# Performance work log

Measured on AMD Instinct MI355X. Metric: run time of the kernel, lower is better.

The kernel has to match this reference:

```python
import jax, jax.numpy as jnp
import numpy as np

EPS = 1e-3  # Keras BatchNormalization default epsilon


def _bn(x, gamma, beta, mean, var):
    # inference-mode batchnorm over channel axis 1 of [N,C,T,V]
    s = (gamma * jax.lax.rsqrt(var + EPS)).reshape(1, -1, 1, 1)
    b = (beta - gamma * mean * jax.lax.rsqrt(var + EPS)).reshape(1, -1, 1, 1)
    return x * s + b


def setup_inputs() -> dict:
    key = jax.random.key(0)
    ks = jax.random.split(key, 10)
    N, C, T, V, K, F, KT = 64, 64, 300, 25, 3, 64, 9
    x = jax.random.normal(ks[0], (N, C, T, V), jnp.float32)
    W1 = jax.random.normal(ks[1], (C, F * K), jnp.float32) * 0.05
    b1 = jnp.zeros((F * K,), jnp.float32)
    A = jax.random.normal(ks[2], (K, T, V, V), jnp.float32) * 0.2
    gamma1 = jnp.ones((F,), jnp.float32)
    beta1 = jnp.zeros((F,), jnp.float32)
    mean1 = jax.random.normal(ks[3], (F,), jnp.float32) * 0.1
    var1 = jax.random.uniform(ks[4], (F,), jnp.float32) + 0.5
    Wt = jax.random.normal(ks[5], (KT, 1, F, F), jnp.float32) * 0.05  # HWIO
    bt = jnp.zeros((F,), jnp.float32)
    gamma2 = jnp.ones((F,), jnp.float32)
    beta2 = jnp.zeros((F,), jnp.float32)
    mean2 = jax.random.normal(ks[6], (F,), jnp.float32) * 0.1
    var2 = jax.random.uniform(ks[7], (F,), jnp.float32) + 0.5
    return dict(x=x, W1=W1, b1=b1, A=A, gamma1=gamma1, beta1=beta1,
                mean1=mean1, var1=var1, Wt=Wt, bt=bt, gamma2=gamma2,
                beta2=beta2, mean2=mean2, var2=var2)


def reference(x, W1, b1, A, gamma1, beta1, mean1, var1, Wt, bt,
              gamma2, beta2, mean2, var2):
    N, C, T, V = x.shape
    K = A.shape[0]
    F = W1.shape[1] // K
    # SGTACN: 1x1 conv (channels_first) == channel matmul
    y = jnp.einsum('nctv,cf->nftv', x, W1) + b1.reshape(1, -1, 1, 1)
    y = y.reshape(N, K, F, T, V)
    # spatial graph contraction with learned per-timestep adjacency
    y = jnp.einsum('nkftv,ktvw->nftw', y, A)
    # tgcn: BN -> relu -> temporal conv [9,1] SAME -> BN
    y = jax.nn.relu(_bn(y, gamma1, beta1, mean1, var1))
    y = jax.lax.conv_general_dilated(
        y, Wt, window_strides=(1, 1), padding='SAME',
        dimension_numbers=('NCHW', 'HWIO', 'NCHW')) + bt.reshape(1, -1, 1, 1)
    y = _bn(y, gamma2, beta2, mean2, var2)
    # identity residual (stride=1, no downsample, C_in == filters) + relu
    return jax.nn.relu(y + x)
```

## Files before the change

### kernel.cpp

```cpp
#include <hip/hip_runtime.h>
#include <hip/hip_bf16.h>
#include <stdint.h>

#define EPS 1e-3f

typedef __attribute__((ext_vector_type(8))) short bf16x8;
typedef __attribute__((ext_vector_type(4))) float f32x4;

__device__ inline uint32_t pk2(float a, float b) {
    __hip_bfloat162 p;
    p.x = __float2bfloat16(a);
    p.y = __float2bfloat16(b);
    return *(uint32_t*)&p;
}

__global__ __launch_bounds__(256) void k0_prep_small(
    const float* __restrict__ W1, const float* __restrict__ Wt,
    const float* __restrict__ A,
    uint16_t* __restrict__ W1t, uint16_t* __restrict__ Abf,
    float* __restrict__ csA_g)
{
    int i = blockIdx.x * 256 + threadIdx.x;
    if (i < 12288) {
        int f = i / 192, Kp = i % 192, k = Kp >> 6, c = Kp & 63;
        __hip_bfloat16 b = __float2bfloat16(W1[c * 192 + k * 64 + f]);
        W1t[i] = *(uint16_t*)&b;
    } else if (i < 49152) {
        int j = i - 12288;
        int jj = j & 7, fo = (j >> 3) & 63, kb = j >> 9;
        int kk = kb * 8 + jj, dt = kk >> 6, fi = kk & 63;
        __hip_bfloat16 b = __float2bfloat16(Wt[(dt * 64 + fi) * 64 + fo]);
        Abf[j] = *(uint16_t*)&b;
    } else if (i < 71652) {
        int j = i - 49152;
        int k = j / 7500, r = j % 7500;
        int t = r / 25, w = r % 25;
        float s = 0.f;
        for (int v = 0; v < 25; ++v)
            s += A[((k * 300 + t) * 25 + v) * 25 + w];
        csA_g[j] = s;
    }
}

__global__ __launch_bounds__(256) void k0_prep_At(
    const float* __restrict__ A, uint16_t* __restrict__ At_g)
{
    int i = blockIdx.x * 256 + threadIdx.x;
    if (i < 921600) {
        int v = i & 31, w = (i >> 5) & 31, rest = i >> 10;
        int t = rest % 300, k = rest / 300;
        float val = 0.f;
        if (v < 25 && w < 25)
            val = A[((k * 300 + t) * 25 + v) * 25 + w];
        __hip_bfloat16 b = __float2bfloat16(val);
        At_g[i] = *(uint16_t*)&b;
    }
}

#define K1_SMEM 39680
__global__ __launch_bounds__(256, 4) void k1_wave(
    const float* __restrict__ x, const uint16_t* __restrict__ At_g,
    const uint16_t* __restrict__ W1t, const float* __restrict__ csA_g,
    const float* __restrict__ b1,
    const float* __restrict__ gamma1, const float* __restrict__ beta1,
    const float* __restrict__ mean1, const float* __restrict__ var1,
    uint32_t* __restrict__ h2u)
{
    extern __shared__ __align__(16) char smem[];
    float* s1s   = (float*)(smem + 38400);
    float* b1ns  = (float*)(smem + 38656);
    float* b1s   = (float*)(smem + 38912);

    const int t0   = blockIdx.x * 4;
    const int n    = blockIdx.y;
    const int tid  = threadIdx.x;
    const int lane = tid & 63, wv = tid >> 6;
    const int l15  = lane & 15, g = lane >> 4;
    const int t    = t0 + wv;
    char* slab = smem + wv * 9600;

    bf16x8 bfr[6];
    #pragma unroll
    for (int nf = 0; nf < 6; ++nf) {
        const int col = nf * 16 + l15;
        const int k = col >> 5, w = col & 31;
        bfr[nf] = *(const bf16x8*)(At_g + (((k * 300 + t) * 32 + w) * 32 + g * 8));
    }

    const float* xb = x + (size_t)n * 480000 + t * 25;
    bf16x8 a[4];
    #pragma unroll
    for (int mf = 0; mf < 4; ++mf) {
        const int c = l15 + 16 * mf;
        const float* xr = xb + (size_t)c * 7500;
        union { bf16x8 v; uint32_t u[4]; } ua;
        if (g < 3) {
            const float* p = xr + g * 8;
            ua.u[0] = pk2(p[0], p[1]);
            ua.u[1] = pk2(p[2], p[3]);
            ua.u[2] = pk2(p[4], p[5]);
            ua.u[3] = pk2(p[6], p[7]);
        } else {
            ua.u[0] = pk2(xr[24], 0.f);
            ua.u[1] = 0; ua.u[2] = 0; ua.u[3] = 0;
        }
        a[mf] = ua.v;
    }

    if (tid < 64) {
        float rs = rsqrtf(var1[tid] + EPS);
        s1s[tid]  = gamma1[tid] * rs;
        b1ns[tid] = beta1[tid] - gamma1[tid] * mean1[tid] * rs;
    }
    if (tid >= 64 && tid < 256) b1s[tid - 64] = b1[tid - 64];
    __syncthreads();

    #pragma unroll
    for (int hh = 0; hh < 2; ++hh) {
        f32x4 acc[4][3];
        #pragma unroll
        for (int mf = 0; mf < 4; ++mf)
            #pragma unroll
            for (int nf3 = 0; nf3 < 3; ++nf3)
                acc[mf][nf3] = (f32x4){0.f, 0.f, 0.f, 0.f};

        #pragma unroll
        for (int nf3 = 0; nf3 < 3; ++nf3) {
            const int nf = hh * 3 + nf3;
            acc[0][nf3] = __builtin_amdgcn_mfma_f32_16x16x32_bf16(a[0], bfr[nf], acc[0][nf3], 0, 0, 0);
            acc[1][nf3] = __builtin_amdgcn_mfma_f32_16x16x32_bf16(a[1], bfr[nf], acc[1][nf3], 0, 0, 0);
            acc[2][nf3] = __builtin_amdgcn_mfma_f32_16x16x32_bf16(a[2], bfr[nf], acc[2][nf3], 0, 0, 0);
            acc[3][nf3] = __builtin_amdgcn_mfma_f32_16x16x32_bf16(a[3], bfr[nf], acc[3][nf3], 0, 0, 0);
        }

        #pragma unroll
        for (int nf3 = 0; nf3 < 3; ++nf3) {
            const int col = (hh * 3 + nf3) * 16 + l15;
            const int k = col >> 5, w = col & 31;
            if (w < 25) {
                const int sw = (w & 7) << 4;
                #pragma unroll
                for (int mf = 0; mf < 4; ++mf) {
                    const int c0 = mf * 16 + g * 4;
                    const int off = w * 384 + (((k * 64 + c0) * 2) ^ sw);
                    uint2 val;
                    val.x = pk2(acc[mf][nf3][0], acc[mf][nf3][1]);
                    val.y = pk2(acc[mf][nf3][2], acc[mf][nf3][3]);
                    *(uint2*)(slab + off) = val;
                }
            }
        }
    }

    asm volatile("s_waitcnt lgkmcnt(0)" ::: "memory");
    __builtin_amdgcn_sched_barrier(0);

    int wq[2], qaddr[2], qswz[2];
    #pragma unroll
    for (int q = 0; q < 2; ++q) {
        int w = q * 16 + l15;
        wq[q] = w;
        int wc = (w < 25) ? w : 24;
        qaddr[q] = wc * 384;
        qswz[q]  = (wc & 7) << 4;
    }

    f32x4 accz[4][2];
    #pragma unroll
    for (int mf = 0; mf < 4; ++mf)
        #pragma unroll
        for (int q = 0; q < 2; ++q)
            accz[mf][q] = (f32x4){0.f, 0.f, 0.f, 0.f};

    #pragma unroll
    for (int kb = 0; kb < 6; ++kb) {
        bf16x8 az[4];
        #pragma unroll
        for (int mf = 0; mf < 4; ++mf)
            az[mf] = *(const bf16x8*)(W1t + (l15 + 16 * mf) * 192 + kb * 32 + g * 8);
        #pragma unroll
        for (int q = 0; q < 2; ++q) {
            bf16x8 b = *(const bf16x8*)(slab + qaddr[q] + ((kb * 64 + g * 16) ^ qswz[q]));
            accz[0][q] = __builtin_amdgcn_mfma_f32_16x16x32_bf16(az[0], b, accz[0][q], 0, 0, 0);
            accz[1][q] = __builtin_amdgcn_mfma_f32_16x16x32_bf16(az[1], b, accz[1][q], 0, 0, 0);
            accz[2][q] = __builtin_amdgcn_mfma_f32_16x16x32_bf16(az[2], b, accz[2][q], 0, 0, 0);
            accz[3][q] = __builtin_amdgcn_mfma_f32_16x16x32_bf16(az[3], b, accz[3][q], 0, 0, 0);
        }
    }

    const uint32_t tb = (uint32_t)(n * 300 + t);
    #pragma unroll
    for (int q = 0; q < 2; ++q) {
        const int w = wq[q];
        if (w < 25) {
            const int ci = t * 25 + w;
            const float cs0 = csA_g[ci];
            const float cs1 = csA_g[7500 + ci];
            const float cs2 = csA_g[15000 + ci];
            const uint32_t rowbase = tb * 800 + w * 32;
            #pragma unroll
            for (int mf = 0; mf < 4; ++mf) {
                const int f0 = mf * 16 + g * 4;
                float zz[4];
                #pragma unroll
                for (int rg = 0; rg < 4; ++rg) {
                    const int f = f0 + rg;
                    float z = accz[mf][q][rg]
                            + b1s[f] * cs0 + b1s[64 + f] * cs1 + b1s[128 + f] * cs2;
                    z = z * s1s[f] + b1ns[f];
                    zz[rg] = fmaxf(z, 0.f);
                }
                uint2 st;
                st.x = pk2(zz[0], zz[1]);
                st.y = pk2(zz[2], zz[3]);
                *(uint2*)(h2u + rowbase + (f0 >> 1)) = st;
            }
        }
    }
}

#define K2_SMEM 51712
__global__ __launch_bounds__(256, 3) void k2_mfma(
    const char* __restrict__ h2b,
    const uint16_t* __restrict__ Abf,
    const float* __restrict__ bt,
    const float* __restrict__ gamma2, const float* __restrict__ beta2,
    const float* __restrict__ mean2,  const float* __restrict__ var2,
    const float* __restrict__ x,
    float* __restrict__ out)
{
    extern __shared__ __align__(16) char smem2[];
    char*  lds_h = smem2;
    float* s2s   = (float*)(smem2 + 51200);
    float* b2s   = s2s + 64;

    const int t0  = blockIdx.x * 8;
    const int n   = blockIdx.y;
    const int tid = threadIdx.x;

    if (tid < 64) {
        float rs = rsqrtf(var2[tid] + EPS);
        float s  = gamma2[tid] * rs;
        s2s[tid] = s;
        b2s[tid] = beta2[tid] - gamma2[tid] * mean2[tid] * rs + bt[tid] * s;
    }

    const size_t hn = (size_t)n * 300 * 3200;
    for (int c = tid; c < 3200; c += 256) {
        int rr = c >> 3, c8 = c & 7;
        int trow = rr / 25;
        int w = rr - trow * 25;
        int tg = t0 - 4 + trow;
        int4 v = make_int4(0, 0, 0, 0);
        if (tg >= 0 && tg < 300)
            v = *(const int4*)(h2b + hn + (size_t)tg * 3200 + w * 128 + (c8 << 4));
        int s = c << 4;
        *(int4*)(lds_h + (s ^ (((s >> 7) & 7) << 4))) = v;
    }
    __syncthreads();

    const int wv = tid >> 6, lane = tid & 63;
    const int l15 = lane & 15, g = lane >> 4;
    const int nMf = (wv == 0) ? 4 : 3;

    int rbase[4];
    #pragma unroll
    for (int q = 0; q < 4; ++q) {
        int col = (q * 4 + wv) * 16 + l15;
        rbase[q] = (col < 200) ? col : 199;
    }

    f32x4 acc[4][4];
    #pragma unroll
    for (int q = 0; q < 4; ++q)
        #pragma unroll
        for (int mf = 0; mf < 4; ++mf)
            acc[q][mf] = (f32x4){0.f, 0.f, 0.f, 0.f};

    for (int kk = 0; kk < 18; ++kk) {
        const int dt   = kk >> 1;
        const int half = (kk & 1) << 6;
        const int kb   = kk * 4 + g;
        bf16x8 wfr[4];
        #pragma unroll
        for (int mf = 0; mf < 4; ++mf)
            wfr[mf] = *(const bf16x8*)(Abf + (kb * 64 + l15 + mf * 16) * 8);
        #pragma unroll
        for (int q = 0; q < 4; ++q) {
            if (q < nMf) {
                int r = rbase[q] + 25 * dt;
                int s = (r << 7) + half + (g << 4);
                bf16x8 hfr = *(const bf16x8*)(lds_h + (s ^ ((r & 7) << 4)));
                acc[q][0] = __builtin_amdgcn_mfma_f32_16x16x32_bf16(hfr, wfr[0], acc[q][0], 0, 0, 0);
                acc[q][1] = __builtin_amdgcn_mfma_f32_16x16x32_bf16(hfr, wfr[1], acc[q][1], 0, 0, 0);
                acc[q][2] = __builtin_amdgcn_mfma_f32_16x16x32_bf16(hfr, wfr[2], acc[q][2], 0, 0, 0);
                acc[q][3] = __builtin_amdgcn_mfma_f32_16x16x32_bf16(hfr, wfr[3], acc[q][3], 0, 0, 0);
            }
        }
    }

    const size_t outn = (size_t)n * 480000;
    const int base = t0 * 25;
    const int vcols = (7500 - base < 200) ? (7500 - base) : 200;
    #pragma unroll
    for (int q = 0; q < 4; ++q) {
        if (q < nMf) {
            const int col0 = (q * 4 + wv) * 16 + g * 4;
            if (col0 < vcols) {
                #pragma unroll
                for (int mf = 0; mf < 4; ++mf) {
                    const int fo = mf * 16 + l15;
                    const size_t ga = outn + (size_t)fo * 7500 + base + col0;
                    const float4 xr = *(const float4*)(x + ga);
                    const float s2 = s2s[fo], b2 = b2s[fo];
                    float4 o;
                    o.x = fmaxf(acc[q][mf][0] * s2 + b2 + xr.x, 0.f);
                    o.y = fmaxf(acc[q][mf][1] * s2 + b2 + xr.y, 0.f);
                    o.z = fmaxf(acc[q][mf][2] * s2 + b2 + xr.z, 0.f);
                    o.w = fmaxf(acc[q][mf][3] * s2 + b2 + xr.w, 0.f);
                    *(float4*)(out + ga) = o;
                }
            }
        }
    }
}

extern "C" void kernel_launch(void* const* d_in, const int* in_sizes, int n_in,
                              void* d_out, int out_size, void* d_ws, size_t ws_size,
                              hipStream_t stream) {
    const float* x      = (const float*)d_in[0];
    const float* W1     = (const float*)d_in[1];
    const float* b1     = (const float*)d_in[2];
    const float* A      = (const float*)d_in[3];
    const float* gamma1 = (const float*)d_in[4];
    const float* beta1  = (const float*)d_in[5];
    const float* mean1  = (const float*)d_in[6];
    const float* var1   = (const float*)d_in[7];
    const float* Wt     = (const float*)d_in[8];
    const float* bt     = (const float*)d_in[9];
    const float* gamma2 = (const float*)d_in[10];
    const float* beta2  = (const float*)d_in[11];
    const float* mean2  = (const float*)d_in[12];
    const float* var2   = (const float*)d_in[13];
    float* out = (float*)d_out;

    char* ws = (char*)d_ws;
    uint32_t* h2u   = (uint32_t*)ws;
    char*     h2b   = ws;
    uint16_t* At_g  = (uint16_t*)(ws + 61440000);
    uint16_t* W1t   = (uint16_t*)(ws + 63283200);
    uint16_t* Abf   = (uint16_t*)(ws + 63307776);
    float*    csA_g = (float*)   (ws + 63381504);

    hipFuncSetAttribute((const void*)k1_wave,
                        hipFuncAttributeMaxDynamicSharedMemorySize, K1_SMEM);
    hipFuncSetAttribute((const void*)k2_mfma,
                        hipFuncAttributeMaxDynamicSharedMemorySize, K2_SMEM);

    k0_prep_small<<<280, 256, 0, stream>>>(W1, Wt, A, W1t, Abf, csA_g);
    k0_prep_At<<<3600, 256, 0, stream>>>(A, At_g);
    k1_wave<<<dim3(75, 64), 256, K1_SMEM, stream>>>(
        x, At_g, W1t, csA_g, b1, gamma1, beta1, mean1, var1, h2u);
    k2_mfma<<<dim3(38, 64), 256, K2_SMEM, stream>>>(
        h2b, Abf, bt, gamma2, beta2, mean2, var2, x, out);
}
```

Baseline: 418.2 us.

## Batch global loads ahead of use and software-prefetch weight fragments in both kernels

In the first kernel, x rows and the csA values are loaded into registers before the setup barrier, and W1t fragments are double-buffered across the kb loop. In the second kernel, the h2 tile is gathered into 13 registers per thread before any LDS stores, A weight fragments are prefetched one step ahead, and residual x values are loaded in a batch before the epilogue. The aim is to put more memory requests in flight and hide global-load latency behind the MFMA work. The cost is higher register pressure, which could reduce occupancy under launch_bounds(256,3) or cause spills.

New measurement: 402.7 us. -3.7%, faster.

```diff
diff --git a/kernel.cpp b/kernel.cpp
--- a/kernel.cpp
+++ b/kernel.cpp
@@ -88,24 +88,33 @@
     }
 
     const float* xb = x + (size_t)n * 480000 + t * 25;
-    bf16x8 a[4];
+    float xr8[4][8];
+    float x24v[4];
     #pragma unroll
     for (int mf = 0; mf < 4; ++mf) {
         const int c = l15 + 16 * mf;
         const float* xr = xb + (size_t)c * 7500;
-        union { bf16x8 v; uint32_t u[4]; } ua;
         if (g < 3) {
             const float* p = xr + g * 8;
-            ua.u[0] = pk2(p[0], p[1]);
-            ua.u[1] = pk2(p[2], p[3]);
-            ua.u[2] = pk2(p[4], p[5]);
-            ua.u[3] = pk2(p[6], p[7]);
+            #pragma unroll
+            for (int j = 0; j < 8; ++j) xr8[mf][j] = p[j];
         } else {
-            ua.u[0] = pk2(xr[24], 0.f);
-            ua.u[1] = 0; ua.u[2] = 0; ua.u[3] = 0;
-        }
-        a[mf] = ua.v;
-    }
+            x24v[mf] = xr[24];
+        }
+    }
+
+    float cs[2][3];
+    #pragma unroll
+    for (int q = 0; q < 2; ++q) {
+        const int w = q * 16 + l15;
+        const int wc = (w < 25) ? w : 24;
+        const int ci = t * 25 + wc;
+        cs[q][0] = csA_g[ci];
+        cs[q][1] = csA_g[7500 + ci];
+        cs[q][2] = csA_g[15000 + ci];
+    }
+
+    __builtin_amdgcn_sched_barrier(0);
 
     if (tid < 64) {
         float rs = rsqrtf(var1[tid] + EPS);
@@ -114,6 +123,22 @@
     }
     if (tid >= 64 && tid < 256) b1s[tid - 64] = b1[tid - 64];
     __syncthreads();
+
+    bf16x8 a[4];
+    #pragma unroll
+    for (int mf = 0; mf < 4; ++mf) {
+        union { bf16x8 v; uint32_t u[4]; } ua;
+        if (g < 3) {
+            ua.u[0] = pk2(xr8[mf][0], xr8[mf][1]);
+            ua.u[1] = pk2(xr8[mf][2], xr8[mf][3]);
+            ua.u[2] = pk2(xr8[mf][4], xr8[mf][5]);
+            ua.u[3] = pk2(xr8[mf][6], xr8[mf][7]);
+        } else {
+            ua.u[0] = pk2(x24v[mf], 0.f);
+            ua.u[1] = 0; ua.u[2] = 0; ua.u[3] = 0;
+        }
+        a[mf] = ua.v;
+    }
 
     #pragma unroll
     for (int hh = 0; hh < 2; ++hh) {
@@ -152,6 +177,11 @@
         }
     }
 
+    bf16x8 azc[4];
+    #pragma unroll
+    for (int mf = 0; mf < 4; ++mf)
+        azc[mf] = *(const bf16x8*)(W1t + (l15 + 16 * mf) * 192 + g * 8);
+
     asm volatile("s_waitcnt lgkmcnt(0)" ::: "memory");
     __builtin_amdgcn_sched_barrier(0);
 
@@ -174,17 +204,23 @@
 
     #pragma unroll
     for (int kb = 0; kb < 6; ++kb) {
-        bf16x8 az[4];
-        #pragma unroll
-        for (int mf = 0; mf < 4; ++mf)
-            az[mf] = *(const bf16x8*)(W1t + (l15 + 16 * mf) * 192 + kb * 32 + g * 8);
+        bf16x8 azn[4];
+        if (kb < 5) {
+            #pragma unroll
+            for (int mf = 0; mf < 4; ++mf)
+                azn[mf] = *(const bf16x8*)(W1t + (l15 + 16 * mf) * 192 + (kb + 1) * 32 + g * 8);
+        }
         #pragma unroll
         for (int q = 0; q < 2; ++q) {
             bf16x8 b = *(const bf16x8*)(slab + qaddr[q] + ((kb * 64 + g * 16) ^ qswz[q]));
-            accz[0][q] = __builtin_amdgcn_mfma_f32_16x16x32_bf16(az[0], b, accz[0][q], 0, 0, 0);
-            accz[1][q] = __builtin_amdgcn_mfma_f32_16x16x32_bf16(az[1], b, accz[1][q], 0, 0, 0);
-            accz[2][q] = __builtin_amdgcn_mfma_f32_16x16x32_bf16(az[2], b, accz[2][q], 0, 0, 0);
-            accz[3][q] = __builtin_amdgcn_mfma_f32_16x16x32_bf16(az[3], b, accz[3][q], 0, 0, 0);
+            accz[0][q] = __builtin_amdgcn_mfma_f32_16x16x32_bf16(azc[0], b, accz[0][q], 0, 0, 0);
+            accz[1][q] = __builtin_amdgcn_mfma_f32_16x16x32_bf16(azc[1], b, accz[1][q], 0, 0, 0);
+            accz[2][q] = __builtin_amdgcn_mfma_f32_16x16x32_bf16(azc[2], b, accz[2][q], 0, 0, 0);
+            accz[3][q] = __builtin_amdgcn_mfma_f32_16x16x32_bf16(azc[3], b, accz[3][q], 0, 0, 0);
+        }
+        if (kb < 5) {
+            #pragma unroll
+            for (int mf = 0; mf < 4; ++mf) azc[mf] = azn[mf];
         }
     }
 
@@ -193,10 +229,6 @@
     for (int q = 0; q < 2; ++q) {
         const int w = wq[q];
         if (w < 25) {
-            const int ci = t * 25 + w;
-            const float cs0 = csA_g[ci];
-            const float cs1 = csA_g[7500 + ci];
-            const float cs2 = csA_g[15000 + ci];
             const uint32_t rowbase = tb * 800 + w * 32;
             #pragma unroll
             for (int mf = 0; mf < 4; ++mf) {
@@ -206,7 +238,8 @@
                 for (int rg = 0; rg < 4; ++rg) {
                     const int f = f0 + rg;
                     float z = accz[mf][q][rg]
-                            + b1s[f] * cs0 + b1s[64 + f] * cs1 + b1s[128 + f] * cs2;
+                            + b1s[f] * cs[q][0] + b1s[64 + f] * cs[q][1]
+                            + b1s[128 + f] * cs[q][2];
                     z = z * s1s[f] + b1ns[f];
                     zz[rg] = fmaxf(z, 0.f);
                 }
@@ -238,6 +271,23 @@
     const int n   = blockIdx.y;
     const int tid = threadIdx.x;
 
+    const size_t hn = (size_t)n * 300 * 3200;
+    int4 tmp[13];
+    #pragma unroll
+    for (int i = 0; i < 13; ++i) {
+        const int c = tid + i * 256;
+        tmp[i] = make_int4(0, 0, 0, 0);
+        if (c < 3200) {
+            int rr = c >> 3, c8 = c & 7;
+            int trow = rr / 25;
+            int w = rr - trow * 25;
+            int tg = t0 - 4 + trow;
+            if (tg >= 0 && tg < 300)
+                tmp[i] = *(const int4*)(h2b + hn + (size_t)tg * 3200 + w * 128 + (c8 << 4));
+        }
+    }
+    __builtin_amdgcn_sched_barrier(0);
+
     if (tid < 64) {
         float rs = rsqrtf(var2[tid] + EPS);
         float s  = gamma2[tid] * rs;
@@ -245,17 +295,13 @@
         b2s[tid] = beta2[tid] - gamma2[tid] * mean2[tid] * rs + bt[tid] * s;
     }
 
-    const size_t hn = (size_t)n * 300 * 3200;
-    for (int c = tid; c < 3200; c += 256) {
-        int rr = c >> 3, c8 = c & 7;
-        int trow = rr / 25;
-        int w = rr - trow * 25;
-        int tg = t0 - 4 + trow;
-        int4 v = make_int4(0, 0, 0, 0);
-        if (tg >= 0 && tg < 300)
-            v = *(const int4*)(h2b + hn + (size_t)tg * 3200 + w * 128 + (c8 << 4));
-        int s = c << 4;
-        *(int4*)(lds_h + (s ^ (((s >> 7) & 7) << 4))) = v;
+    #pragma unroll
+    for (int i = 0; i < 13; ++i) {
+        const int c = tid + i * 256;
+        if (c < 3200) {
+            int s = c << 4;
+            *(int4*)(lds_h + (s ^ (((s >> 7) & 7) << 4))) = tmp[i];
+        }
     }
     __syncthreads();
 
@@ -277,49 +323,72 @@
         for (int mf = 0; mf < 4; ++mf)
             acc[q][mf] = (f32x4){0.f, 0.f, 0.f, 0.f};
 
+    bf16x8 wc_[4];
+    #pragma unroll
+    for (int mf = 0; mf < 4; ++mf)
+        wc_[mf] = *(const bf16x8*)(Abf + ((0 * 4 + g) * 64 + l15 + mf * 16) * 8);
+
     for (int kk = 0; kk < 18; ++kk) {
         const int dt   = kk >> 1;
         const int half = (kk & 1) << 6;
-        const int kb   = kk * 4 + g;
-        bf16x8 wfr[4];
-        #pragma unroll
-        for (int mf = 0; mf < 4; ++mf)
-            wfr[mf] = *(const bf16x8*)(Abf + (kb * 64 + l15 + mf * 16) * 8);
+        bf16x8 wn_[4];
+        if (kk < 17) {
+            const int kbn = (kk + 1) * 4 + g;
+            #pragma unroll
+            for (int mf = 0; mf < 4; ++mf)
+                wn_[mf] = *(const bf16x8*)(Abf + (kbn * 64 + l15 + mf * 16) * 8);
+        }
         #pragma unroll
         for (int q = 0; q < 4; ++q) {
             if (q < nMf) {
                 int r = rbase[q] + 25 * dt;
                 int s = (r << 7) + half + (g << 4);
                 bf16x8 hfr = *(const bf16x8*)(lds_h + (s ^ ((r & 7) << 4)));
-                acc[q][0] = __builtin_amdgcn_mfma_f32_16x16x32_bf16(hfr, wfr[0], acc[q][0], 0, 0, 0);
-                acc[q][1] = __builtin_amdgcn_mfma_f32_16x16x32_bf16(hfr, wfr[1], acc[q][1], 0, 0, 0);
-                acc[q][2] = __builtin_amdgcn_mfma_f32_16x16x32_bf16(hfr, wfr[2], acc[q][2], 0, 0, 0);
-                acc[q][3] = __builtin_amdgcn_mfma_f32_16x16x32_bf16(hfr, wfr[3], acc[q][3], 0, 0, 0);
+                acc[q][0] = __builtin_amdgcn_mfma_f32_16x16x32_bf16(hfr, wc_[0], acc[q][0], 0, 0, 0);
+                acc[q][1] = __builtin_amdgcn_mfma_f32_16x16x32_bf16(hfr, wc_[1], acc[q][1], 0, 0, 0);
+                acc[q][2] = __builtin_amdgcn_mfma_f32_16x16x32_bf16(hfr, wc_[2], acc[q][2], 0, 0, 0);
+                acc[q][3] = __builtin_amdgcn_mfma_f32_16x16x32_bf16(hfr, wc_[3], acc[q][3], 0, 0, 0);
             }
+        }
+        if (kk < 17) {
+            #pragma unroll
+            for (int mf = 0; mf < 4; ++mf) wc_[mf] = wn_[mf];
         }
     }
 
     const size_t outn = (size_t)n * 480000;
     const int base = t0 * 25;
     const int vcols = (7500 - base < 200) ? (7500 - base) : 200;
+
+    float4 xrv[4][4];
     #pragma unroll
     for (int q = 0; q < 4; ++q) {
-        if (q < nMf) {
-            const int col0 = (q * 4 + wv) * 16 + g * 4;
-            if (col0 < vcols) {
-                #pragma unroll
-                for (int mf = 0; mf < 4; ++mf) {
-                    const int fo = mf * 16 + l15;
-                    const size_t ga = outn + (size_t)fo * 7500 + base + col0;
-                    const float4 xr = *(const float4*)(x + ga);
-                    const float s2 = s2s[fo], b2 = b2s[fo];
-                    float4 o;
-                    o.x = fmaxf(acc[q][mf][0] * s2 + b2 + xr.x, 0.f);
-                    o.y = fmaxf(acc[q][mf][1] * s2 + b2 + xr.y, 0.f);
-                    o.z = fmaxf(acc[q][mf][2] * s2 + b2 + xr.z, 0.f);
-                    o.w = fmaxf(acc[q][mf][3] * s2 + b2 + xr.w, 0.f);
-                    *(float4*)(out + ga) = o;
-                }
+        const int col0 = (q * 4 + wv) * 16 + g * 4;
+        if (q < nMf && col0 < vcols) {
+            #pragma unroll
+            for (int mf = 0; mf < 4; ++mf) {
+                const int fo = mf * 16 + l15;
+                xrv[q][mf] = *(const float4*)(x + outn + (size_t)fo * 7500 + base + col0);
+            }
+        }
+    }
+    __builtin_amdgcn_sched_barrier(0);
+
+    #pragma unroll
+    for (int q = 0; q < 4; ++q) {
+        const int col0 = (q * 4 + wv) * 16 + g * 4;
+        if (q < nMf && col0 < vcols) {
+            #pragma unroll
+            for (int mf = 0; mf < 4; ++mf) {
+                const int fo = mf * 16 + l15;
+                const size_t ga = outn + (size_t)fo * 7500 + base + col0;
+                const float s2 = s2s[fo], b2 = b2s[fo];
+                float4 o;
+                o.x = fmaxf(acc[q][mf][0] * s2 + b2 + xrv[q][mf].x, 0.f);
+                o.y = fmaxf(acc[q][mf][1] * s2 + b2 + xrv[q][mf].y, 0.f);
+                o.z = fmaxf(acc[q][mf][2] * s2 + b2 + xrv[q][mf].z, 0.f);
+                o.w = fmaxf(acc[q][mf][3] * s2 + b2 + xrv[q][mf].w, 0.f);
+                *(float4*)(out + ga) = o;
             }
         }
     }
```
